# Performance work log

Measured on AMD Instinct MI355X. Metric: run time of the kernel, lower is better.

## Reference

```python
import jax, jax.numpy as jnp
import numpy as np

POOL = 7        # output pooled size
SAMP = 2 * POOL # crop_and_resize sampling resolution (14)


def _bilinear_crop(feat, ys, xs):
    """feat [H,W,C]; ys,xs [N,S] sample coords in feature-map pixels -> [N,S,S,C]."""
    H, W, _ = feat.shape
    ys = jnp.clip(ys, 0.0, H - 1.0)
    xs = jnp.clip(xs, 0.0, W - 1.0)
    y0f = jnp.floor(ys); x0f = jnp.floor(xs)
    y0 = y0f.astype(jnp.int32); x0 = x0f.astype(jnp.int32)
    y1 = jnp.clip(y0 + 1, 0, H - 1); x1 = jnp.clip(x0 + 1, 0, W - 1)
    wy = (ys - y0f)[:, :, None, None]   # [N,S,1,1]
    wx = (xs - x0f)[:, None, :, None]   # [N,1,S,1]
    g = lambda yi, xi: feat[yi[:, :, None], xi[:, None, :]]  # [N,S,S,C]
    out = g(y0, x0) * (1 - wy) * (1 - wx)
    out = out + g(y0, x1) * (1 - wy) * wx
    out = out + g(y1, x0) * wy * (1 - wx)
    out = out + g(y1, x1) * wy * wx
    return out


def setup_inputs() -> dict:
    key = jax.random.key(0)
    k1, k2, k3, k4, k5 = jax.random.split(key, 5)
    Hf, Wf, C = 37, 50, 512
    N = 1000
    H_img, W_img = 600.0, 800.0
    inputs = jax.random.normal(k1, (1, Hf, Wf, C), dtype=jnp.float32)
    # random valid boxes (x1,y1,x2,y2) in image coords
    cx = jax.random.uniform(k2, (N,)) * W_img
    cy = jax.random.uniform(k3, (N,)) * H_img
    bw = jax.random.uniform(k4, (N,)) * 300.0 + 16.0
    bh = jax.random.uniform(k5, (N,)) * 300.0 + 16.0
    x1 = jnp.clip(cx - bw / 2, 0.0, W_img - 1.0)
    y1 = jnp.clip(cy - bh / 2, 0.0, H_img - 1.0)
    x2 = jnp.clip(cx + bw / 2, 0.0, W_img - 1.0)
    y2 = jnp.clip(cy + bh / 2, 0.0, H_img - 1.0)
    rois = jnp.stack([x1, y1, x2, y2], axis=1).astype(jnp.float32)
    im_size = jnp.array([600, 800], dtype=jnp.int32)  # (h, w)
    return {"inputs": inputs, "rois": rois, "im_size": im_size}


def reference(inputs, rois, im_size):
    feat = inputs[0]                       # [Hf, Wf, C]
    Hf, Wf, C = feat.shape
    h = im_size[0].astype(jnp.float32)
    w = im_size[1].astype(jnp.float32)
    # normalize boxes to [0,1] (y1, x1, y2, x2), as in roi_pool_tf
    ny1 = rois[:, 1] / h; nx1 = rois[:, 0] / w
    ny2 = rois[:, 3] / h; nx2 = rois[:, 2] / w
    # crop_and_resize sample grid (TF convention: endpoints at box corners)
    t = jnp.linspace(0.0, 1.0, SAMP, dtype=jnp.float32)          # [S]
    ys = (ny1[:, None] + (ny2 - ny1)[:, None] * t[None, :]) * (Hf - 1)  # [N,S]
    xs = (nx1[:, None] + (nx2 - nx1)[:, None] * t[None, :]) * (Wf - 1)  # [N,S]
    crops = _bilinear_crop(feat, ys, xs)   # [N,14,14,C]
    N = crops.shape[0]
    pooled = crops.reshape(N, POOL, 2, POOL, 2, C).max(axis=(2, 4))  # [N,7,7,C]
    return pooled
```

## Files before the change

kernel.cpp:

```cpp
#include <hip/hip_runtime.h>
#include <math.h>

#define HF 37
#define WF 50
#define CC 512
#define POOLD 7
#define SAMPD 14

typedef float nfloat4 __attribute__((ext_vector_type(4)));

__device__ __forceinline__ float4 lerp4(float4 a, float4 b, float t) {
    float4 r;
    r.x = a.x + t * (b.x - a.x);
    r.y = a.y + t * (b.y - a.y);
    r.z = a.z + t * (b.z - a.z);
    r.w = a.w + t * (b.w - a.w);
    return r;
}

__device__ __forceinline__ float4 max4(float4 a, float4 b) {
    float4 r;
    r.x = fmaxf(a.x, b.x);
    r.y = fmaxf(a.y, b.y);
    r.z = fmaxf(a.z, b.z);
    r.w = fmaxf(a.w, b.w);
    return r;
}

__device__ __forceinline__ void store_nt4(float* p, float4 v) {
    nfloat4 nv;
    nv.x = v.x; nv.y = v.y; nv.z = v.z; nv.w = v.w;
    __builtin_nontemporal_store(nv, (nfloat4*)p);
}

struct Raw { float4 a, b, c, d; };

template <int RC>
__device__ __forceinline__ Raw loadraw(const float* __restrict__ pbase, int col,
                                       int ro0, int ro1, int ro2, int ro3) {
    const float* p = pbase + (size_t)col * CC;
    Raw r;
    r.a = *(const float4*)(p + ro0);
    r.b = *(const float4*)(p + ro1);
    if (RC == 1) { r.c = *(const float4*)(p + ro3); }
    if (RC == 2) { r.c = *(const float4*)(p + ro2); r.d = *(const float4*)(p + ro3); }
    return r;
}

template <int RC>
__device__ __forceinline__ void vlerp(const Raw& r, float wya, float wyb,
                                      float4& va, float4& vb) {
    if (RC == 0)      { va = lerp4(r.a, r.b, wya); vb = lerp4(r.a, r.b, wyb); }
    else if (RC == 1) { va = lerp4(r.a, r.b, wya); vb = lerp4(r.b, r.c, wyb); }
    else              { va = lerp4(r.a, r.b, wya); vb = lerp4(r.c, r.d, wyb); }
}

template <int RC>
__device__ __forceinline__ void run_row(const float* __restrict__ pbase,
                                        float4* __restrict__ lbase,
                                        float nx1, float dx,
                                        int ro0, int ro1, int ro2, int ro3,
                                        float wya, float wyb)
{
    const float inv    = 1.0f / (float)(SAMPD - 1);
    const float wscale = (float)(WF - 1);

    auto samp = [&](int sx, int& pc, float& w) {
        float tx = (float)sx * inv;
        float xs = fmaf(dx, tx, nx1) * wscale;
        xs = fminf(fmaxf(xs, 0.0f), wscale);
        float x0f = floorf(xs);
        int ci = (int)x0f;
        float wx = xs - x0f;
        if (ci >= WF - 1) { pc = WF - 1; w = 1.0f; }
        else              { pc = ci + 1; w = wx; }
        pc = __builtin_amdgcn_readfirstlane(pc);
    };

    int pc0, pcl; float w0, wl;
    samp(0, pc0, w0);
    samp(SAMPD - 1, pcl, wl);
    int cfirst = pc0 - 1;
    int clast  = pcl;

    Raw r0 = loadraw<RC>(pbase, cfirst, ro0, ro1, ro2, ro3);
    Raw rA = loadraw<RC>(pbase, cfirst + 1, ro0, ro1, ro2, ro3);
    Raw rB;
    float4 vaP, vbP;
    vlerp<RC>(r0, wya, wyb, vaP, vbP);

    float4 m0 = make_float4(-INFINITY, -INFINITY, -INFINITY, -INFINITY);
    int sx = 0;
    int c  = cfirst + 1;

    auto consume = [&](float4 vaC, float4 vbC) {
        for (;;) {
            if (sx >= SAMPD) break;
            int pc; float w;
            samp(sx, pc, w);
            if (pc > c) break;
            float4 sa = lerp4(vaP, vaC, w);
            float4 sb = lerp4(vbP, vbC, w);
            m0 = max4(m0, max4(sa, sb));
            if (sx & 1) {
                lbase[(sx >> 1) * 128] = m0;
                m0 = make_float4(-INFINITY, -INFINITY, -INFINITY, -INFINITY);
            }
            ++sx;
        }
        vaP = vaC; vbP = vbC;
    };

    for (;;) {
        {
            int cn = min(c + 1, clast);
            rB = loadraw<RC>(pbase, cn, ro0, ro1, ro2, ro3);
            float4 vaC, vbC;
            vlerp<RC>(rA, wya, wyb, vaC, vbC);
            consume(vaC, vbC);
            if (c == clast) return;
            ++c;
        }
        {
            int cn = min(c + 1, clast);
            rA = loadraw<RC>(pbase, cn, ro0, ro1, ro2, ro3);
            float4 vaC, vbC;
            vlerp<RC>(rB, wya, wyb, vaC, vbC);
            consume(vaC, vbC);
            if (c == clast) return;
            ++c;
        }
    }
}

__global__ __launch_bounds__(128, 4) void roipool_kernel(
    const float* __restrict__ feat,
    const float* __restrict__ rois,
    const int*   __restrict__ im_size,
    float*       __restrict__ out,
    int N)
{
    __shared__ float4 lds_out[POOLD * 128];

    int bid = blockIdx.x;
    int n   = bid / POOLD;
    int py  = bid - n * POOLD;
    if (n >= N) return;

    float h = (float)im_size[0];
    float w = (float)im_size[1];
    float4 box = *(const float4*)(rois + 4 * n);
    float ny1 = box.y / h, nx1 = box.x / w;
    float ny2 = box.w / h, nx2 = box.z / w;
    float dx = nx2 - nx1;

    const float inv = 1.0f / (float)(SAMPD - 1);

    float tya = (float)(2 * py) * inv;
    float tyb = (float)(2 * py + 1) * inv;
    float ysa = (ny1 + (ny2 - ny1) * tya) * (float)(HF - 1);
    float ysb = (ny1 + (ny2 - ny1) * tyb) * (float)(HF - 1);
    ysa = fminf(fmaxf(ysa, 0.0f), (float)(HF - 1));
    ysb = fminf(fmaxf(ysb, 0.0f), (float)(HF - 1));
    float y0fa = floorf(ysa);
    float y0fb = floorf(ysb);
    float wya = ysa - y0fa;
    float wyb = ysb - y0fb;
    int iya = __builtin_amdgcn_readfirstlane((int)y0fa);
    int iyb = __builtin_amdgcn_readfirstlane((int)y0fb);
    int iya1 = min(iya + 1, HF - 1);
    int iyb1 = min(iyb + 1, HF - 1);
    int ro0 = iya  * (WF * CC);
    int ro1 = iya1 * (WF * CC);
    int ro2 = iyb  * (WF * CC);
    int ro3 = iyb1 * (WF * CC);

    const float* pbase = feat + (size_t)threadIdx.x * 4;
    float4* lbase = lds_out + threadIdx.x;
    float* obase = out + ((size_t)(n * POOLD + py) * POOLD) * CC + (size_t)threadIdx.x * 4;

    if (ro2 == ro0) {
        run_row<0>(pbase, lbase, nx1, dx, ro0, ro1, ro2, ro3, wya, wyb);
    } else if (ro2 == ro1) {
        run_row<1>(pbase, lbase, nx1, dx, ro0, ro1, ro2, ro3, wya, wyb);
    } else {
        run_row<2>(pbase, lbase, nx1, dx, ro0, ro1, ro2, ro3, wya, wyb);
    }

    #pragma unroll
    for (int p = 0; p < POOLD; ++p) {
        float4 v = lbase[p * 128];
        store_nt4(obase + (size_t)p * CC, v);
    }
}

extern "C" void kernel_launch(void* const* d_in, const int* in_sizes, int n_in,
                              void* d_out, int out_size, void* d_ws, size_t ws_size,
                              hipStream_t stream) {
    const float* feat    = (const float*)d_in[0];
    const float* rois    = (const float*)d_in[1];
    const int*   im_size = (const int*)d_in[2];
    float* out = (float*)d_out;

    int N = in_sizes[1] / 4;
    int nblocks = N * POOLD;
    roipool_kernel<<<nblocks, 128, 0, stream>>>(feat, rois, im_size, out, N);
}
```

Baseline: 126.9 us.

## Replace column-walk loop with fully unrolled per-sample software-pipelined loads

The data-dependent walk over feature columns, which reused each loaded column across samples, is replaced by a fully unrolled loop over the 14 x samples. Each sample loads both of its neighbouring columns, with a prefetch depth that depends on how many distinct rows the case needs. Pooled results are also stored straight to global memory, dropping the LDS staging buffer. Control flow becomes static and memory-level parallelism rises, at the cost of redundant column loads (roughly twice as many), more registers and possibly lower occupancy.

Result: slower. 136.5 us (+7.6%).

```diff
diff --git a/kernel.cpp b/kernel.cpp
--- a/kernel.cpp
+++ b/kernel.cpp
@@ -57,78 +57,48 @@
 
 template <int RC>
 __device__ __forceinline__ void run_row(const float* __restrict__ pbase,
-                                        float4* __restrict__ lbase,
+                                        float* __restrict__ obase,
                                         float nx1, float dx,
                                         int ro0, int ro1, int ro2, int ro3,
                                         float wya, float wyb)
 {
     const float inv    = 1.0f / (float)(SAMPD - 1);
     const float wscale = (float)(WF - 1);
+    constexpr int D     = (RC == 0) ? 3 : ((RC == 1) ? 2 : 1);
+    constexpr int SLOTS = D + 1;
 
-    auto samp = [&](int sx, int& pc, float& w) {
-        float tx = (float)sx * inv;
-        float xs = fmaf(dx, tx, nx1) * wscale;
-        xs = fminf(fmaxf(xs, 0.0f), wscale);
-        float x0f = floorf(xs);
-        int ci = (int)x0f;
-        float wx = xs - x0f;
-        if (ci >= WF - 1) { pc = WF - 1; w = 1.0f; }
-        else              { pc = ci + 1; w = wx; }
-        pc = __builtin_amdgcn_readfirstlane(pc);
-    };
-
-    int pc0, pcl; float w0, wl;
-    samp(0, pc0, w0);
-    samp(SAMPD - 1, pcl, wl);
-    int cfirst = pc0 - 1;
-    int clast  = pcl;
-
-    Raw r0 = loadraw<RC>(pbase, cfirst, ro0, ro1, ro2, ro3);
-    Raw rA = loadraw<RC>(pbase, cfirst + 1, ro0, ro1, ro2, ro3);
-    Raw rB;
-    float4 vaP, vbP;
-    vlerp<RC>(r0, wya, wyb, vaP, vbP);
+    Raw   ls[SLOTS], rs[SLOTS];
+    float ws[SLOTS];
 
     float4 m0 = make_float4(-INFINITY, -INFINITY, -INFINITY, -INFINITY);
-    int sx = 0;
-    int c  = cfirst + 1;
 
-    auto consume = [&](float4 vaC, float4 vbC) {
-        for (;;) {
-            if (sx >= SAMPD) break;
-            int pc; float w;
-            samp(sx, pc, w);
-            if (pc > c) break;
-            float4 sa = lerp4(vaP, vaC, w);
-            float4 sb = lerp4(vbP, vbC, w);
+    #pragma unroll
+    for (int i = 0; i < SAMPD + D; ++i) {
+        if (i < SAMPD) {
+            float tx  = (float)i * inv;
+            float xs  = fmaf(dx, tx, nx1) * wscale;
+            xs        = fminf(fmaxf(xs, 0.0f), wscale);
+            float x0f = floorf(xs);
+            int c0 = __builtin_amdgcn_readfirstlane((int)x0f);
+            int c1 = min(c0 + 1, WF - 1);
+            ws[i % SLOTS] = xs - x0f;
+            ls[i % SLOTS] = loadraw<RC>(pbase, c0, ro0, ro1, ro2, ro3);
+            rs[i % SLOTS] = loadraw<RC>(pbase, c1, ro0, ro1, ro2, ro3);
+        }
+        if (i >= D) {
+            int k = i - D;
+            int s = k % SLOTS;
+            float4 va0, vb0, va1, vb1;
+            vlerp<RC>(ls[s], wya, wyb, va0, vb0);
+            vlerp<RC>(rs[s], wya, wyb, va1, vb1);
+            float w  = ws[s];
+            float4 sa = lerp4(va0, va1, w);
+            float4 sb = lerp4(vb0, vb1, w);
             m0 = max4(m0, max4(sa, sb));
-            if (sx & 1) {
-                lbase[(sx >> 1) * 128] = m0;
+            if (k & 1) {
+                store_nt4(obase + (size_t)(k >> 1) * CC, m0);
                 m0 = make_float4(-INFINITY, -INFINITY, -INFINITY, -INFINITY);
             }
-            ++sx;
-        }
-        vaP = vaC; vbP = vbC;
-    };
-
-    for (;;) {
-        {
-            int cn = min(c + 1, clast);
-            rB = loadraw<RC>(pbase, cn, ro0, ro1, ro2, ro3);
-            float4 vaC, vbC;
-            vlerp<RC>(rA, wya, wyb, vaC, vbC);
-            consume(vaC, vbC);
-            if (c == clast) return;
-            ++c;
-        }
-        {
-            int cn = min(c + 1, clast);
-            rA = loadraw<RC>(pbase, cn, ro0, ro1, ro2, ro3);
-            float4 vaC, vbC;
-            vlerp<RC>(rB, wya, wyb, vaC, vbC);
-            consume(vaC, vbC);
-            if (c == clast) return;
-            ++c;
         }
     }
 }
@@ -140,8 +110,6 @@
     float*       __restrict__ out,
     int N)
 {
-    __shared__ float4 lds_out[POOLD * 128];
-
     int bid = blockIdx.x;
     int n   = bid / POOLD;
     int py  = bid - n * POOLD;
@@ -176,21 +144,14 @@
     int ro3 = iyb1 * (WF * CC);
 
     const float* pbase = feat + (size_t)threadIdx.x * 4;
-    float4* lbase = lds_out + threadIdx.x;
     float* obase = out + ((size_t)(n * POOLD + py) * POOLD) * CC + (size_t)threadIdx.x * 4;
 
     if (ro2 == ro0) {
-        run_row<0>(pbase, lbase, nx1, dx, ro0, ro1, ro2, ro3, wya, wyb);
+        run_row<0>(pbase, obase, nx1, dx, ro0, ro1, ro2, ro3, wya, wyb);
     } else if (ro2 == ro1) {
-        run_row<1>(pbase, lbase, nx1, dx, ro0, ro1, ro2, ro3, wya, wyb);
+        run_row<1>(pbase, obase, nx1, dx, ro0, ro1, ro2, ro3, wya, wyb);
     } else {
-        run_row<2>(pbase, lbase, nx1, dx, ro0, ro1, ro2, ro3, wya, wyb);
-    }
-
-    #pragma unroll
-    for (int p = 0; p < POOLD; ++p) {
-        float4 v = lbase[p * 128];
-        store_nt4(obase + (size_t)p * CC, v);
+        run_row<2>(pbase, obase, nx1, dx, ro0, ro1, ro2, ro3, wya, wyb);
     }
 }
 
```
